# Kernel tuning notes

Measured on AMD Instinct MI355X. Metric: run time of the kernel, lower is better.

## Reference

```python
import jax, jax.numpy as jnp
import numpy as np

B, L, E, D, A = 128, 1024, 512, 512, 512


def setup_inputs() -> dict:
    key = jax.random.key(0)
    ks = jax.random.split(key, 8)
    s_e = 1.0 / np.sqrt(E)
    s_d = 1.0 / np.sqrt(D)
    s_a = 1.0 / np.sqrt(A)
    return {
        "encoder_out": jax.random.normal(ks[0], (B, L, E), jnp.float32),
        "decoder_hidden": jax.random.normal(ks[1], (B, D), jnp.float32),
        "W_enc": jax.random.uniform(ks[2], (E, A), jnp.float32, -s_e, s_e),
        "b_enc": jax.random.uniform(ks[3], (A,), jnp.float32, -s_e, s_e),
        "W_dec": jax.random.uniform(ks[4], (D, A), jnp.float32, -s_d, s_d),
        "b_dec": jax.random.uniform(ks[5], (A,), jnp.float32, -s_d, s_d),
        "W_full": jax.random.uniform(ks[6], (A,), jnp.float32, -s_a, s_a),
        "b_full": jax.random.uniform(ks[7], (), jnp.float32, -s_a, s_a),
    }


def reference(encoder_out, decoder_hidden, W_enc, b_enc, W_dec, b_dec, W_full, b_full):
    # att1: [B, L, A]; att2: [B, A]
    att1 = jnp.einsum('ble,ea->bla', encoder_out, W_enc) + b_enc
    att2 = jnp.einsum('bd,da->ba', decoder_hidden, W_dec) + b_dec
    # scores: [B, L] -- ReLU(att1 + att2[:, None]) projected to scalar
    att = jnp.einsum('bla,a->bl', jax.nn.relu(att1 + att2[:, None, :]), W_full) + b_full
    alpha = jax.nn.softmax(att, axis=1)  # softmax over positions
    # weighted sum over positions: [B, E]
    weighted = jnp.einsum('ble,bl->be', encoder_out, alpha)
    return weighted, alpha
```

## Files before the change

### kernel.cpp

```cpp
#include <hip/hip_runtime.h>

#define NB 128
#define NL 1024
#define NE 512
#define NA 512
#define ND 512

typedef __attribute__((ext_vector_type(8))) short short8;
typedef __attribute__((ext_vector_type(4))) float f32x4;

static __device__ __forceinline__ unsigned short f2bf(float f) {
  unsigned int u = __float_as_uint(f);
  u += 0x7FFF + ((u >> 16) & 1);
  return (unsigned short)(u >> 16);
}

__global__ void k_prep(const float* __restrict__ W_enc,
                       unsigned short* __restrict__ Bpack,
                       const float* __restrict__ dec,
                       const float* __restrict__ Wdec,
                       const float* __restrict__ b_enc,
                       const float* __restrict__ b_dec,
                       float* __restrict__ att2) {
  int blk = blockIdx.x;
  int tid = threadIdx.x;
  if (blk < 64) {
    int t = blk * 512 + tid;
    int lane = t & 63;
    int rest = t >> 6;
    int nf = rest & 31;
    int ki = rest >> 5;
    int col = nf * 16 + (lane & 15);
    int kbase = ki * 32 + (lane >> 4) * 8;
    short8 v;
#pragma unroll
    for (int j = 0; j < 8; ++j)
      v[j] = (short)f2bf(W_enc[(kbase + j) * NA + col]);
    *reinterpret_cast<short8*>(Bpack + (long)t * 8) = v;
  } else {
    int b = blk - 64;
    int a = tid;
    float acc = b_enc[a] + b_dec[a];
    const float* drow = dec + b * ND;
#pragma unroll 8
    for (int d = 0; d < ND; ++d)
      acc += drow[d] * Wdec[d * NA + a];
    att2[b * NA + a] = acc;
  }
}

__global__ __attribute__((amdgpu_waves_per_eu(4))) __launch_bounds__(512)
void k_main(const float* __restrict__ enc,
            const unsigned short* __restrict__ Bpack,
            const float* __restrict__ att2g, const float* __restrict__ wfull,
            float* __restrict__ attg, float* __restrict__ ogp,
            float* __restrict__ mzg) {
  extern __shared__ char smem[];
  const int t = threadIdx.x;
  const int lane = t & 63;
  const int wave = t >> 6;
  const int l15 = lane & 15;
  const int lq = lane >> 4;
  const int blk = blockIdx.x;
  const int batch = blk >> 4;
  const long row0 = (long)blk * 64;
  const int srow16 = t >> 4;
  const int scol8 = t & 15;

#define G_LOAD(Q, FI, GA, GB)                                                 \
  {                                                                           \
    int row = (FI)*32 + srow16;                                               \
    const float* src = enc + (row0 + row) * NE + (Q)*128 + scol8 * 8;         \
    GA = *reinterpret_cast<const float4*>(src);                               \
    GB = *reinterpret_cast<const float4*>(src + 4);                           \
  }
#define G_WRITE(Q, FI, GA, GB)                                                \
  {                                                                           \
    int row = (FI)*32 + srow16;                                               \
    short8 o;                                                                 \
    o[0] = (short)f2bf(GA.x); o[1] = (short)f2bf(GA.y);                       \
    o[2] = (short)f2bf(GA.z); o[3] = (short)f2bf(GA.w);                       \
    o[4] = (short)f2bf(GB.x); o[5] = (short)f2bf(GB.y);                       \
    o[6] = (short)f2bf(GB.z); o[7] = (short)f2bf(GB.w);                       \
    int byt = (row * 1024 + (Q)*256 + scol8 * 16) ^ ((row & 7) << 4);         \
    *reinterpret_cast<short8*>(smem + byt) = o;                               \
  }

  {
    float4 h[8];
#pragma unroll
    for (int c = 0; c < 4; ++c) {
      int q = c >> 1;
      int row = (c & 1) * 32 + srow16;
      const float* src = enc + (row0 + row) * NE + q * 128 + scol8 * 8;
      h[c * 2] = *reinterpret_cast<const float4*>(src);
      h[c * 2 + 1] = *reinterpret_cast<const float4*>(src + 4);
    }
#pragma unroll
    for (int c = 0; c < 4; ++c) {
      int q = c >> 1;
      int row = (c & 1) * 32 + srow16;
      float4 xa = h[c * 2], xb = h[c * 2 + 1];
      short8 o;
      o[0] = (short)f2bf(xa.x); o[1] = (short)f2bf(xa.y);
      o[2] = (short)f2bf(xa.z); o[3] = (short)f2bf(xa.w);
      o[4] = (short)f2bf(xb.x); o[5] = (short)f2bf(xb.y);
      o[6] = (short)f2bf(xb.z); o[7] = (short)f2bf(xb.w);
      int byt = (row * 1024 + q * 256 + scol8 * 16) ^ ((row & 7) << 4);
      *reinterpret_cast<short8*>(smem + byt) = o;
    }
  }
  __syncthreads();

  f32x4 acc[4][4];
#pragma unroll
  for (int rt = 0; rt < 4; ++rt)
#pragma unroll
    for (int cf = 0; cf < 4; ++cf) acc[rt][cf] = (f32x4){0.f, 0.f, 0.f, 0.f};

  const short8* bp = reinterpret_cast<const short8*>(Bpack);
#define K_STEP(KI)                                                            \
  {                                                                           \
    short8 bv0 = bp[((KI)*32 + wave * 4 + 0) * 64 + lane];                    \
    short8 bv1 = bp[((KI)*32 + wave * 4 + 1) * 64 + lane];                    \
    short8 bv2 = bp[((KI)*32 + wave * 4 + 2) * 64 + lane];                    \
    short8 bv3 = bp[((KI)*32 + wave * 4 + 3) * 64 + lane];                    \
    _Pragma("unroll") for (int rt = 0; rt < 4; ++rt) {                        \
      int row = rt * 16 + l15;                                                \
      int byt = (row * 1024 + (KI)*64 + lq * 16) ^ ((row & 7) << 4);          \
      short8 av = *reinterpret_cast<const short8*>(smem + byt);               \
      acc[rt][0] = __builtin_amdgcn_mfma_f32_16x16x32_bf16(av, bv0, acc[rt][0], 0, 0, 0); \
      acc[rt][1] = __builtin_amdgcn_mfma_f32_16x16x32_bf16(av, bv1, acc[rt][1], 0, 0, 0); \
      acc[rt][2] = __builtin_amdgcn_mfma_f32_16x16x32_bf16(av, bv2, acc[rt][2], 0, 0, 0); \
      acc[rt][3] = __builtin_amdgcn_mfma_f32_16x16x32_bf16(av, bv3, acc[rt][3], 0, 0, 0); \
    }                                                                         \
  }

  {
    float4 g0, g1, g2, g3;
    G_LOAD(2, 0, g0, g1) K_STEP(0)
    G_LOAD(2, 1, g2, g3) K_STEP(1)
    G_WRITE(2, 0, g0, g1) K_STEP(2)
    G_WRITE(2, 1, g2, g3) K_STEP(3)
    G_LOAD(3, 0, g0, g1) K_STEP(4)
    G_LOAD(3, 1, g2, g3) K_STEP(5)
    G_WRITE(3, 0, g0, g1) K_STEP(6)
    G_WRITE(3, 1, g2, g3) K_STEP(7)
  }
  __syncthreads();
  K_STEP(8)  K_STEP(9)  K_STEP(10) K_STEP(11)
  K_STEP(12) K_STEP(13) K_STEP(14) K_STEP(15)
#undef K_STEP
#undef G_LOAD
#undef G_WRITE

  float a2r[4], wfr[4];
#pragma unroll
  for (int cf = 0; cf < 4; ++cf) {
    int col = wave * 64 + cf * 16 + l15;
    a2r[cf] = att2g[batch * NA + col];
    wfr[cf] = wfull[col];
  }
  float px[4][4];
#pragma unroll
  for (int rt = 0; rt < 4; ++rt)
#pragma unroll
    for (int r = 0; r < 4; ++r) px[rt][r] = 0.f;
#pragma unroll
  for (int cf = 0; cf < 4; ++cf) {
#pragma unroll
    for (int rt = 0; rt < 4; ++rt)
#pragma unroll
      for (int r = 0; r < 4; ++r) {
        float v = acc[rt][cf][r] + a2r[cf];
        px[rt][r] += fmaxf(v, 0.f) * wfr[cf];
      }
  }
#pragma unroll
  for (int rt = 0; rt < 4; ++rt)
#pragma unroll
    for (int r = 0; r < 4; ++r) {
      float p_ = px[rt][r];
      p_ += __shfl_xor(p_, 1);
      p_ += __shfl_xor(p_, 2);
      p_ += __shfl_xor(p_, 4);
      p_ += __shfl_xor(p_, 8);
      px[rt][r] = p_;
    }
  float* red = (float*)(smem + 65536);
  float* pl = (float*)(smem + 65536 + 2048);
  if (l15 == 0) {
#pragma unroll
    for (int rt = 0; rt < 4; ++rt)
#pragma unroll
      for (int r = 0; r < 4; ++r)
        red[wave * 64 + rt * 16 + lq * 4 + r] = px[rt][r];
  }
  __syncthreads();
  float sc = 0.f;
#pragma unroll
  for (int w8 = 0; w8 < 8; ++w8) sc += red[w8 * 64 + lane];
  if (t < 64) attg[blk * 64 + t] = sc;
  float m = sc;
#pragma unroll
  for (int off = 1; off < 64; off <<= 1) m = fmaxf(m, __shfl_xor(m, off));
  float p = expf(sc - m);
  float Z = p;
#pragma unroll
  for (int off = 1; off < 64; off <<= 1) Z += __shfl_xor(Z, off);
  if (t < 64) pl[t] = p;
  __syncthreads();

  {
    int half = t >> 8;
    int e = (t & 255) * 2;
    float o0 = 0.f, o1 = 0.f;
#pragma unroll
    for (int i = 0; i < 32; ++i) {
      int row = half * 32 + i;
      float pw = pl[row];
      int byt = (row * 1024 + e * 2) ^ ((row & 7) << 4);
      unsigned u = *reinterpret_cast<const unsigned*>(smem + byt);
      o0 += pw * __uint_as_float(u << 16);
      o1 += pw * __uint_as_float(u & 0xffff0000u);
    }
    __syncthreads();
    float2* xch = (float2*)red;
    if (half) xch[t - 256] = make_float2(o0, o1);
    __syncthreads();
    if (!half) {
      float2 hv = xch[t];
      *reinterpret_cast<float2*>(ogp + (long)blk * 512 + e) =
          make_float2(o0 + hv.x, o1 + hv.y);
    }
    if (t == 0) {
      mzg[blk * 2] = m;
      mzg[blk * 2 + 1] = Z;
    }
  }
}

__global__ void k_final(const float* __restrict__ attg,
                        const float* __restrict__ ogp,
                        const float* __restrict__ mzg,
                        float* __restrict__ weighted,
                        float* __restrict__ alpha) {
  int b = blockIdx.x;
  int t = threadIdx.x;
  float mv[16], zv[16];
  float m = -__builtin_huge_valf();
#pragma unroll
  for (int i = 0; i < 16; ++i) {
    mv[i] = mzg[(b * 16 + i) * 2];
    zv[i] = mzg[(b * 16 + i) * 2 + 1];
    m = fmaxf(m, mv[i]);
  }
  float Z = 0.f;
#pragma unroll
  for (int i = 0; i < 16; ++i) {
    float s = expf(mv[i] - m);
    mv[i] = s;
    Z += s * zv[i];
  }
  float inv = 1.f / Z;
  float o = 0.f;
#pragma unroll
  for (int i = 0; i < 16; ++i) o += mv[i] * ogp[((long)b * 16 + i) * 512 + t];
  weighted[b * NE + t] = o * inv;
  alpha[b * NL + t] = expf(attg[b * NL + t] - m) * inv;
  alpha[b * NL + 512 + t] = expf(attg[b * NL + 512 + t] - m) * inv;
}

extern "C" void kernel_launch(void* const* d_in, const int* in_sizes, int n_in,
                              void* d_out, int out_size, void* d_ws, size_t ws_size,
                              hipStream_t stream) {
  const float* enc    = (const float*)d_in[0];
  const float* dec    = (const float*)d_in[1];
  const float* W_enc  = (const float*)d_in[2];
  const float* b_enc  = (const float*)d_in[3];
  const float* W_dec  = (const float*)d_in[4];
  const float* b_dec  = (const float*)d_in[5];
  const float* W_full = (const float*)d_in[6];

  float* out = (float*)d_out;
  float* weighted = out;
  float* alpha = out + NB * NE;

  char* ws = (char*)d_ws;
  float* att2          = (float*)ws;
  unsigned short* Bpk  = (unsigned short*)(ws + (256 << 10));
  float* attg          = (float*)(ws + (768 << 10));
  float* ogp           = (float*)(ws + (1280 << 10));
  float* mzg           = (float*)(ws + (5376 << 10));

  hipLaunchKernelGGL(k_prep, dim3(192), dim3(512), 0, stream,
                     W_enc, Bpk, dec, W_dec, b_enc, b_dec, att2);
  hipLaunchKernelGGL(k_main, dim3(2048), dim3(512), 67840, stream,
                     enc, Bpk, att2, W_full, attg, ogp, mzg);
  hipLaunchKernelGGL(k_final, dim3(NB), dim3(512), 0, stream,
                     attg, ogp, mzg, weighted, alpha);
}
```

Before: 123.7 us.

## Pipeline encoder tile loads per K-quarter and stagger start order across blocks

The kernel now loads a single K-quarter of the encoder tile (instead of two) before the first barrier. The remaining quarters are loaded while the MFMA steps for the previous quarter run, with one barrier per quarter. Blocks picked by popcount parity start from the opposite half of K, which spreads concurrent reads of the shared packed weight slices and the encoder columns. The aim is to shorten the exposed load latency at block start, at the cost of more barriers and two code paths.

```diff
diff --git a/kernel.cpp b/kernel.cpp
--- a/kernel.cpp
+++ b/kernel.cpp
@@ -66,6 +66,7 @@
   const long row0 = (long)blk * 64;
   const int srow16 = t >> 4;
   const int scol8 = t & 15;
+  const int phase = __popc(blk) & 1;
 
 #define G_LOAD(Q, FI, GA, GB)                                                 \
   {                                                                           \
@@ -85,32 +86,6 @@
     int byt = (row * 1024 + (Q)*256 + scol8 * 16) ^ ((row & 7) << 4);         \
     *reinterpret_cast<short8*>(smem + byt) = o;                               \
   }
-
-  {
-    float4 h[8];
-#pragma unroll
-    for (int c = 0; c < 4; ++c) {
-      int q = c >> 1;
-      int row = (c & 1) * 32 + srow16;
-      const float* src = enc + (row0 + row) * NE + q * 128 + scol8 * 8;
-      h[c * 2] = *reinterpret_cast<const float4*>(src);
-      h[c * 2 + 1] = *reinterpret_cast<const float4*>(src + 4);
-    }
-#pragma unroll
-    for (int c = 0; c < 4; ++c) {
-      int q = c >> 1;
-      int row = (c & 1) * 32 + srow16;
-      float4 xa = h[c * 2], xb = h[c * 2 + 1];
-      short8 o;
-      o[0] = (short)f2bf(xa.x); o[1] = (short)f2bf(xa.y);
-      o[2] = (short)f2bf(xa.z); o[3] = (short)f2bf(xa.w);
-      o[4] = (short)f2bf(xb.x); o[5] = (short)f2bf(xb.y);
-      o[6] = (short)f2bf(xb.z); o[7] = (short)f2bf(xb.w);
-      int byt = (row * 1024 + q * 256 + scol8 * 16) ^ ((row & 7) << 4);
-      *reinterpret_cast<short8*>(smem + byt) = o;
-    }
-  }
-  __syncthreads();
 
   f32x4 acc[4][4];
 #pragma unroll
@@ -136,23 +111,47 @@
     }                                                                         \
   }
 
-  {
-    float4 g0, g1, g2, g3;
-    G_LOAD(2, 0, g0, g1) K_STEP(0)
-    G_LOAD(2, 1, g2, g3) K_STEP(1)
-    G_WRITE(2, 0, g0, g1) K_STEP(2)
-    G_WRITE(2, 1, g2, g3) K_STEP(3)
-    G_LOAD(3, 0, g0, g1) K_STEP(4)
-    G_LOAD(3, 1, g2, g3) K_STEP(5)
-    G_WRITE(3, 0, g0, g1) K_STEP(6)
-    G_WRITE(3, 1, g2, g3) K_STEP(7)
-  }
+#define PRO(Q)                                                                \
+  {                                                                           \
+    float4 h0, h1, h2, h3;                                                    \
+    G_LOAD(Q, 0, h0, h1)                                                      \
+    G_LOAD(Q, 1, h2, h3)                                                      \
+    G_WRITE(Q, 0, h0, h1)                                                     \
+    G_WRITE(Q, 1, h2, h3)                                                     \
+  }
+#define FOUR(KB, QS)                                                          \
+  {                                                                           \
+    float4 g0, g1, g2, g3;                                                    \
+    G_LOAD(QS, 0, g0, g1) K_STEP((KB) + 0)                                    \
+    G_LOAD(QS, 1, g2, g3) K_STEP((KB) + 1)                                    \
+    G_WRITE(QS, 0, g0, g1) K_STEP((KB) + 2)                                   \
+    G_WRITE(QS, 1, g2, g3) K_STEP((KB) + 3)                                   \
+  }                                                                           \
   __syncthreads();
-  K_STEP(8)  K_STEP(9)  K_STEP(10) K_STEP(11)
-  K_STEP(12) K_STEP(13) K_STEP(14) K_STEP(15)
+#define LAST(KB)                                                              \
+  K_STEP((KB) + 0) K_STEP((KB) + 1) K_STEP((KB) + 2) K_STEP((KB) + 3)
+
+  if (phase == 0) {
+    PRO(0)
+    __syncthreads();
+    FOUR(0, 1)
+    FOUR(4, 2)
+    FOUR(8, 3)
+    LAST(12)
+  } else {
+    PRO(2)
+    __syncthreads();
+    FOUR(8, 3)
+    FOUR(12, 0)
+    FOUR(0, 1)
+    LAST(4)
+  }
 #undef K_STEP
 #undef G_LOAD
 #undef G_WRITE
+#undef PRO
+#undef FOUR
+#undef LAST
 
   float a2r[4], wfr[4];
 #pragma unroll
```

After: 128.4 us. 3.8% more time.
